# Performance work log

Measured on AMD Instinct MI355X. Metric: run time of the kernel, lower is better.

The kernel has to match this reference:

```python
import jax, jax.numpy as jnp
import numpy as np

B, T, S = 128, 256, 64
IN, H, K, CSL, OUT = 3, 512, 10, 60, 121


def setup_inputs() -> dict:
    key = jax.random.key(0)
    ks = jax.random.split(key, 10)
    s = lambda k, shape, sc: jax.random.normal(k, shape, jnp.float32) * sc
    return {
        "x": jax.random.normal(ks[0], (B, T, IN), jnp.float32),
        "sentences": jax.random.uniform(ks[1], (B, S, CSL), dtype=jnp.float32),
        "h1_h": jnp.zeros((B, H), jnp.float32),
        "h1_c": jnp.zeros((B, H), jnp.float32),
        "h2_h": jnp.zeros((B, H), jnp.float32),
        "h2_c": jnp.zeros((B, H), jnp.float32),
        # LSTMCell params (torch gate order i,f,g,o); b = b_ih + b_hh fused
        "W_ih_cell": s(ks[2], (4 * H, IN + CSL), 0.04),
        "W_hh_cell": s(ks[3], (4 * H, H), 0.04),
        "b_cell": jnp.zeros((4 * H,), jnp.float32),
        # second-layer nn.LSTM params
        "W_ih_l": s(ks[4], (4 * H, IN + CSL + H), 0.04),
        "W_hh_l": s(ks[5], (4 * H, H), 0.04),
        "b_l": jnp.zeros((4 * H,), jnp.float32),
        # fc1 -> window params, fc2 -> output
        "W1": s(ks[6], (3 * K, H), 0.04),
        "b1": jnp.zeros((3 * K,), jnp.float32),
        "W2": s(ks[7], (OUT, H), 0.04),
        "b2": jnp.zeros((OUT,), jnp.float32),
    }


def _lstm_step(h, c, xt, W_ih, W_hh, b):
    g = xt @ W_ih.T + h @ W_hh.T + b
    i, f, gg, o = jnp.split(g, 4, axis=-1)
    c2 = jax.nn.sigmoid(f) * c + jax.nn.sigmoid(i) * jnp.tanh(gg)
    h2 = jax.nn.sigmoid(o) * jnp.tanh(c2)
    return h2, c2


def reference(x, sentences, h1_h, h1_c, h2_h, h2_c,
              W_ih_cell, W_hh_cell, b_cell,
              W_ih_l, W_hh_l, b_l, W1, b1, W2, b2):
    u = jnp.arange(1, S + 1, dtype=x.dtype)[:, None]  # [S,1] char positions

    def step1(carry, xt):
        h, c, p = carry
        ip = jnp.exp(h @ W1.T + b1)                                     # [B,3K]
        # kappa part subtracts the previous step's kappa (quirk of the source)
        p_new = jnp.concatenate([ip[:, :2 * K], ip[:, 2 * K:] - p[:, 2 * K:]], axis=-1)
        a, be, ka = jnp.split(p_new[:, None, :], 3, axis=-1)            # each [B,1,K]
        phi = (a * jnp.exp(-be * (ka - u) ** 2)).sum(-1)                # [B,S]
        win = jnp.einsum('bs,bsc->bc', phi, sentences)                  # [B,CSL]
        h2, c2 = _lstm_step(h, c, jnp.concatenate([xt, win], axis=-1),
                            W_ih_cell, W_hh_cell, b_cell)
        return (h2, c2, p_new), (h2, win)

    xs = jnp.swapaxes(x, 0, 1)                                          # [T,B,IN]
    p0 = jnp.zeros((x.shape[0], 3 * K), x.dtype)
    (h1f, c1f, _), (hx, wins) = jax.lax.scan(step1, (h1_h, h1_c, p0), xs)

    feat = jnp.concatenate([xs, wins, hx], axis=-1)                     # [T,B,IN+CSL+H]

    def step2(carry, xt):
        h, c = carry
        h2, c2 = _lstm_step(h, c, xt, W_ih_l, W_hh_l, b_l)
        return (h2, c2), h2

    (h2f, c2f), ys = jax.lax.scan(step2, (h2_h, h2_c), feat)
    y = jnp.swapaxes(ys, 0, 1).reshape(-1, H)                           # [B*T,H]
    out = y @ W2.T + b2                                                 # [B*T,OUT]
    return out, h1f, c1f, h2f, c2f
```

## Files before the change

kernel.cpp:

```cpp
#include <hip/hip_runtime.h>
#include <hip/hip_bf16.h>
#include <math.h>

typedef __attribute__((ext_vector_type(8))) short short8;
typedef __attribute__((ext_vector_type(4))) float floatx4;

#define DEVFN static __device__ __forceinline__

constexpr int B = 128, T = 256, H = 512;
constexpr int OUTW = 121;
constexpr int SLOTW = 1664;
constexpr int LOOF  = 1088;
constexpr int SLOTE = B * SLOTW;
constexpr int NSLOT = T + 2;
constexpr int NG  = 2048;
constexpr int K1  = 576,  K1C = 18;
constexpr int K2  = 1088, K2C = 34;
constexpr int KW1P = 584, KW2P = 1096;

constexpr int O_WH1 = 0;
constexpr int O_WL1 = 37376;
constexpr int O_W1S = 74752;
constexpr int O_GSM = 137152;
constexpr int O_HS  = 137152;
constexpr int O_PP  = 139264;
constexpr int O_IPL = 145472;
constexpr int O_KL  = 145592;
constexpr int O_PHL = 145632;
constexpr int O_WAC = 145888;
constexpr int O_KPR = 146848;
constexpr int O_B1S = 146888;
constexpr int O_BIA = 147008;
constexpr int O_SENT = 147136;
constexpr int O_WH2 = 0;
constexpr int O_WL2 = 70144;
constexpr int O_GS2 = 140288;
constexpr int O_BI2 = 148608;
constexpr int LDS_SZ = 162496;

DEVFN __hip_bfloat16 bhi(float v) { return __float2bfloat16(v); }
DEVFN __hip_bfloat16 blo(float v, __hip_bfloat16 h) { return __float2bfloat16(v - __bfloat162float(h)); }
DEVFN float bf2f(__hip_bfloat16 h) { return __bfloat162float(h); }
DEVFN unsigned short bbits(__hip_bfloat16 h) { union { __hip_bfloat16 h; unsigned short u; } c; c.h = h; return c.u; }
DEVFN unsigned int pack2(float a, float b) {
  return (unsigned int)bbits(bhi(a)) | ((unsigned int)bbits(bhi(b)) << 16);
}
DEVFN void ast(unsigned int* p, unsigned int v) {
  __hip_atomic_store(p, v, __ATOMIC_RELAXED, __HIP_MEMORY_SCOPE_AGENT);
}
DEVFN int ald(int* p) {
  return __hip_atomic_load(p, __ATOMIC_RELAXED, __HIP_MEMORY_SCOPE_AGENT);
}

DEVFN void waitcnt_ge(int* cnt, int target) {
  if (threadIdx.x == 0) {
    int g = 0;
    while (ald(cnt) < target && g < (1 << 24)) { ++g; __builtin_amdgcn_s_sleep(1); }
  }
  asm volatile("" ::: "memory");
  __syncthreads();
}
DEVFN void cnt_add(int* cnt) {
  asm volatile("s_waitcnt vmcnt(0)" ::: "memory");
  __syncthreads();
  if (threadIdx.x == 0)
    (void)__hip_atomic_fetch_add(cnt, 1, __ATOMIC_RELAXED, __HIP_MEMORY_SCOPE_AGENT);
}

__global__ __launch_bounds__(256) void k_pre(
    const float* __restrict__ x, const float* __restrict__ h1h, const float* __restrict__ h2h,
    const float* __restrict__ Wihc, const float* __restrict__ Whhc, const float* __restrict__ bc,
    const float* __restrict__ Wihl, const float* __restrict__ Whhl, const float* __restrict__ bl,
    const float* __restrict__ W2,
    __hip_bfloat16* __restrict__ fxHL,
    __hip_bfloat16* __restrict__ wc1, __hip_bfloat16* __restrict__ wc1l,
    __hip_bfloat16* __restrict__ wc2, __hip_bfloat16* __restrict__ wc2l,
    __hip_bfloat16* __restrict__ w2b, float* __restrict__ bi1, float* __restrict__ bi2,
    int* __restrict__ ctl)
{
  int idx = blockIdx.x * 256 + threadIdx.x;
  const int nwc1 = NG * K1, nwc2 = NG * K2, nw2b = 128 * 512, nbi = 2 * NG;
  const int nfh = B * H, nxj = T * B, nctl = 512;
  if (idx < nwc1) {
    int n = idx / K1, col = idx - n * K1;
    int src = (n & 3) * H + (n >> 2);
    float v = (col < 63) ? Wihc[src * 63 + col]
            : (col == 63 ? 0.f : Whhc[src * 512 + (col - 64)]);
    __hip_bfloat16 h = bhi(v);
    wc1[n * K1 + col] = h; wc1l[n * K1 + col] = blo(v, h);
    return;
  }
  idx -= nwc1;
  if (idx < nwc2) {
    int n = idx / K2, col = idx - n * K2;
    int src = (n & 3) * H + (n >> 2);
    float v;
    if (col < 63)       v = Wihl[src * 575 + col];
    else if (col == 63) v = 0.f;
    else if (col < 576) v = Wihl[src * 575 + (col - 1)];
    else                v = Whhl[src * 512 + (col - 576)];
    __hip_bfloat16 h = bhi(v);
    wc2[n * K2 + col] = h; wc2l[n * K2 + col] = blo(v, h);
    return;
  }
  idx -= nwc2;
  if (idx < nw2b) {
    int n = idx >> 9, col = idx & 511;
    w2b[idx] = bhi(n < OUTW ? W2[n * 512 + col] : 0.f);
    return;
  }
  idx -= nw2b;
  if (idx < nbi) {
    int n = idx & (NG - 1);
    int src = (n & 3) * H + (n >> 2);
    if (idx < NG) bi1[n] = bc[src]; else bi2[n] = bl[src];
    return;
  }
  idx -= nbi;
  if (idx < nfh) {
    int b = idx >> 9, j = idx & 511;
    float v = h1h[idx];
    __hip_bfloat16 h = bhi(v);
    fxHL[b * SLOTW + 64 + j] = h;
    fxHL[b * SLOTW + LOOF + 64 + j] = blo(v, h);
    return;
  }
  idx -= nfh;
  if (idx < nfh) {
    int b = idx >> 9, j = idx & 511;
    fxHL[(size_t)SLOTE + b * SLOTW + 576 + j] = bhi(h2h[idx]);
    return;
  }
  idx -= nfh;
  if (idx < nxj) {
    int t = idx >> 7, b = idx & 127;
    float x0 = x[(b * T + t) * 3 + 0], x1 = x[(b * T + t) * 3 + 1];
    unsigned int* ph = (unsigned int*)(fxHL + (size_t)(t + 1) * SLOTE + b * SLOTW);
    ph[0] = pack2(x0, x1);
    unsigned int* pl = (unsigned int*)(fxHL + (size_t)(t + 1) * SLOTE + b * SLOTW + LOOF);
    pl[0] = 0u;
    return;
  }
  idx -= nxj;
  if (idx < nctl) ctl[idx] = 0;
}

template <int KWP>
DEVFN void gemm3(int tid, const __hip_bfloat16* __restrict__ Aslot, int m0,
                 const __hip_bfloat16* __restrict__ Wh, const __hip_bfloat16* __restrict__ Wl,
                 int cbeg, int cend, floatx4& a0, floatx4& a1)
{
  const int lane = tid & 63, wv = tid >> 6;
  const int lm = lane & 15, lk = (lane >> 4) << 3;
  const __hip_bfloat16* Ar = Aslot + (size_t)(m0 + wv * 16 + lm) * SLOTW;
  const __hip_bfloat16* W0h = Wh + lm * KWP;
  const __hip_bfloat16* W1h = Wh + (16 + lm) * KWP;
  const __hip_bfloat16* W0l = Wl + lm * KWP;
  const __hip_bfloat16* W1l = Wl + (16 + lm) * KWP;
  #pragma unroll 4
  for (int c = cbeg; c < cend; ++c) {
    int col = c * 32 + lk;
    short8 va  = *(const short8*)(Ar + col);
    short8 ua  = *(const short8*)(Ar + LOOF + col);
    short8 vb0 = *(const short8*)(W0h + col);
    short8 vb1 = *(const short8*)(W1h + col);
    short8 ub0 = *(const short8*)(W0l + col);
    short8 ub1 = *(const short8*)(W1l + col);
    a0 = __builtin_amdgcn_mfma_f32_16x16x32_bf16(va, vb0, a0, 0, 0, 0);
    a1 = __builtin_amdgcn_mfma_f32_16x16x32_bf16(va, vb1, a1, 0, 0, 0);
    a0 = __builtin_amdgcn_mfma_f32_16x16x32_bf16(va, ub0, a0, 0, 0, 0);
    a1 = __builtin_amdgcn_mfma_f32_16x16x32_bf16(va, ub1, a1, 0, 0, 0);
    a0 = __builtin_amdgcn_mfma_f32_16x16x32_bf16(ua, vb0, a0, 0, 0, 0);
    a1 = __builtin_amdgcn_mfma_f32_16x16x32_bf16(ua, vb1, a1, 0, 0, 0);
  }
}

DEVFN void store_gsm(int tid, float* Gsm, floatx4 a0, floatx4 a1) {
  const int lane = tid & 63, wv = tid >> 6;
  const int lm = lane & 15, rr = (lane >> 4) << 2;
  #pragma unroll
  for (int r = 0; r < 4; ++r) {
    Gsm[lm * 65 + wv * 16 + rr + r]        = a0[r];
    Gsm[(16 + lm) * 65 + wv * 16 + rr + r] = a1[r];
  }
}

__global__ __launch_bounds__(256, 1) void k_persist(
    __hip_bfloat16* __restrict__ fxHL,
    const __hip_bfloat16* __restrict__ wc1, const __hip_bfloat16* __restrict__ wc1l,
    const __hip_bfloat16* __restrict__ wc2, const __hip_bfloat16* __restrict__ wc2l,
    const float* __restrict__ bi1, const float* __restrict__ bi2,
    const float* __restrict__ c1init, const float* __restrict__ c2init,
    const float* __restrict__ xin, const float* __restrict__ sent,
    const float* __restrict__ W1, const float* __restrict__ b1,
    int* __restrict__ ctl,
    float* __restrict__ h1f, float* __restrict__ c1f,
    float* __restrict__ h2f, float* __restrict__ c2f)
{
  extern __shared__ char sm[];
  const int gid = blockIdx.x, tid = threadIdx.x;
  const int lane = tid & 63, wv = tid >> 6;
  const int lm = lane & 15, lk = (lane >> 4) << 3;

  if (gid < 128) {
    const int nt1 = gid >> 1, mh = gid & 1;
    const int n0 = nt1 * 32, m0 = mh * 64;
    const int brow = mh * 64 + nt1;
    int* hcnt = ctl + mh * 32;
    int* wcnt = ctl + 64 + mh * 32;
    __hip_bfloat16* smWh = (__hip_bfloat16*)(sm + O_WH1);
    __hip_bfloat16* smWl = (__hip_bfloat16*)(sm + O_WL1);
    float* smW1 = (float*)(sm + O_W1S);
    float* Gsm  = (float*)(sm + O_GSM);
    float* hs   = (float*)(sm + O_HS);
    float* winv = (float*)(sm + O_HS);
    float* pp   = (float*)(sm + O_PP);
    float* ipl  = (float*)(sm + O_IPL);
    float* kl   = (float*)(sm + O_KL);
    float* phl  = (float*)(sm + O_PHL);
    float* wac  = (float*)(sm + O_WAC);
    float* kpr  = (float*)(sm + O_KPR);
    float* b1s  = (float*)(sm + O_B1S);
    float* bia  = (float*)(sm + O_BIA);
    float* ssent = (float*)(sm + O_SENT);

    for (int i = tid; i < 32 * 72; i += 256) {
      int r = i / 72, c8 = (i - r * 72) * 8;
      *(short8*)(smWh + r * KW1P + c8) = *(const short8*)(wc1  + (size_t)(n0 + r) * K1 + c8);
      *(short8*)(smWl + r * KW1P + c8) = *(const short8*)(wc1l + (size_t)(n0 + r) * K1 + c8);
    }
    for (int i = tid; i < 30 * 512; i += 256) {
      int j = i >> 9, c = i & 511;
      smW1[j * 520 + (c >> 6) * 65 + (c & 63)] = W1[i];
    }
    for (int i = tid; i < 64 * 60; i += 256)
      ssent[i] = sent[(size_t)brow * 64 * 60 + i];
    if (tid < 30) b1s[tid] = b1[tid];
    if (tid < 10) kpr[tid] = 0.f;
    if (tid < 32) bia[tid] = bi1[n0 + tid];
    __syncthreads();

    float creg[2];
    {
      int ml = tid >> 2, ppi = tid & 3;
      creg[0] = c1init[(m0 + ml) * H + nt1 * 8 + 2 * ppi + 0];
      creg[1] = c1init[(m0 + ml) * H + nt1 * 8 + 2 * ppi + 1];
    }

    const __hip_bfloat16* W0h = smWh + lm * KW1P;
    const __hip_bfloat16* W1h = smWh + (16 + lm) * KW1P;
    const __hip_bfloat16* W0l = smWl + lm * KW1P;
    const __hip_bfloat16* W1l = smWl + (16 + lm) * KW1P;

    for (int t = 0; t < T; ++t) {
      __hip_bfloat16* S1 = fxHL + (size_t)(t + 1) * SLOTE;
      __hip_bfloat16* S0 = fxHL + (size_t)t * SLOTE;

      waitcnt_ge(hcnt, 64 * t);

      const __hip_bfloat16* wrow = S0 + (size_t)brow * SLOTW;
      __hip_bfloat16 a0h = wrow[64 + tid];
      __hip_bfloat16 a0l = wrow[LOOF + 64 + tid];
      __hip_bfloat16 a1h = wrow[64 + 256 + tid];
      __hip_bfloat16 a1l = wrow[LOOF + 64 + 256 + tid];
      float x2v = xin[(brow * T + t) * 3 + 2];
      const __hip_bfloat16* Ar = S0 + (size_t)(m0 + wv * 16 + lm) * SLOTW;
      short8 pva[16], pua[16];
      #pragma unroll
      for (int c = 0; c < 16; ++c) {
        pva[c] = *(const short8*)(Ar + (c + 2) * 32 + lk);
        pua[c] = *(const short8*)(Ar + LOOF + (c + 2) * 32 + lk);
      }
      hs[(tid >> 6) * 66 + (tid & 63)] = bf2f(a0h) + bf2f(a0l);
      hs[((tid + 256) >> 6) * 66 + (tid & 63)] = bf2f(a1h) + bf2f(a1l);
      __syncthreads();

      if (tid < 240) {
        int j = tid >> 3, p = tid & 7;
        const float* wp = smW1 + j * 520 + p * 65;
        const float* hv = hs + p * 66;
        float s = 0.f;
        #pragma unroll 8
        for (int k = 0; k < 64; ++k) s += hv[k] * wp[k];
        pp[tid] = s;
      }
      __syncthreads();
      if (tid < 30) {
        float s = b1s[tid];
        #pragma unroll
        for (int p = 0; p < 8; ++p) s += pp[tid * 8 + p];
        ipl[tid] = expf(s);
      }
      __syncthreads();
      if (tid < 10) {
        float kap = ipl[20 + tid] - kpr[tid];
        kpr[tid] = kap; kl[tid] = kap;
      }
      __syncthreads();
      if (tid < 64) {
        float u = (float)(tid + 1);
        float acc = 0.f;
        #pragma unroll
        for (int k = 0; k < 10; ++k) {
          float d = kl[k] - u;
          acc += ipl[k] * expf(-ipl[10 + k] * d * d);
        }
        phl[tid] = acc;
      }
      __syncthreads();
      if (tid < 240) {
        int c = tid >> 2, p = tid & 3;
        float acc = 0.f;
        #pragma unroll
        for (int s0 = 0; s0 < 16; ++s0)
          acc += phl[p * 16 + s0] * ssent[(p * 16 + s0) * 60 + c];
        wac[tid] = acc;
      }
      __syncthreads();
      if (tid < 60)
        winv[tid] = wac[tid * 4] + wac[tid * 4 + 1] + wac[tid * 4 + 2] + wac[tid * 4 + 3];
      __syncthreads();
      if (tid < 31) {
        int d = 1 + tid;
        int c0 = 2 * d, c1 = 2 * d + 1;
        float v0 = (c0 == 2) ? x2v : winv[c0 - 3];
        float v1 = (c1 == 63) ? 0.f : winv[c1 - 3];
        __hip_bfloat16 h0 = bhi(v0), h1v = bhi(v1);
        unsigned int* prow = (unsigned int*)(S1 + (size_t)brow * SLOTW);
        ast(prow + d, (unsigned int)bbits(h0) | ((unsigned int)bbits(h1v) << 16));
        ast(prow + (LOOF >> 1) + d,
            (unsigned int)bbits(blo(v0, h0)) | ((unsigned int)bbits(blo(v1, h1v)) << 16));
      }
      cnt_add(wcnt);

      floatx4 a0 = {0.f, 0.f, 0.f, 0.f}, a1 = a0;
      #pragma unroll
      for (int c = 0; c < 16; ++c) {
        int col = (c + 2) * 32 + lk;
        short8 vb0 = *(const short8*)(W0h + col);
        short8 vb1 = *(const short8*)(W1h + col);
        short8 ub0 = *(const short8*)(W0l + col);
        short8 ub1 = *(const short8*)(W1l + col);
        a0 = __builtin_amdgcn_mfma_f32_16x16x32_bf16(pva[c], vb0, a0, 0, 0, 0);
        a1 = __builtin_amdgcn_mfma_f32_16x16x32_bf16(pva[c], vb1, a1, 0, 0, 0);
        a0 = __builtin_amdgcn_mfma_f32_16x16x32_bf16(pva[c], ub0, a0, 0, 0, 0);
        a1 = __builtin_amdgcn_mfma_f32_16x16x32_bf16(pva[c], ub1, a1, 0, 0, 0);
        a0 = __builtin_amdgcn_mfma_f32_16x16x32_bf16(pua[c], vb0, a0, 0, 0, 0);
        a1 = __builtin_amdgcn_mfma_f32_16x16x32_bf16(pua[c], vb1, a1, 0, 0, 0);
      }
      waitcnt_ge(wcnt, 64 * (t + 1));
      gemm3<KW1P>(tid, S1, m0, smWh, smWl, 0, 2, a0, a1);
      store_gsm(tid, Gsm, a0, a1);
      __syncthreads();

      {
        int ml = tid >> 2, ppi = tid & 3;
        float v[2];
        #pragma unroll
        for (int j = 0; j < 2; ++j) {
          int nl = ppi * 8 + j * 4;
          float gi = Gsm[(nl + 0) * 65 + ml] + bia[nl + 0];
          float gf = Gsm[(nl + 1) * 65 + ml] + bia[nl + 1];
          float gg = Gsm[(nl + 2) * 65 + ml] + bia[nl + 2];
          float go = Gsm[(nl + 3) * 65 + ml] + bia[nl + 3];
          float ig = 1.f / (1.f + expf(-gi));
          float fg = 1.f / (1.f + expf(-gf));
          float gt = tanhf(gg);
          float og = 1.f / (1.f + expf(-go));
          float cn = fg * creg[j] + ig * gt;
          v[j] = og * tanhf(cn);
          creg[j] = cn;
        }
        __hip_bfloat16 h0 = bhi(v[0]), h1v = bhi(v[1]);
        unsigned int* prow = (unsigned int*)(S1 + (size_t)(m0 + ml) * SLOTW);
        int dw = 32 + nt1 * 4 + ppi;
        ast(prow + dw, (unsigned int)bbits(h0) | ((unsigned int)bbits(h1v) << 16));
        ast(prow + (LOOF >> 1) + dw,
            (unsigned int)bbits(blo(v[0], h0)) | ((unsigned int)bbits(blo(v[1], h1v)) << 16));
        if (t == T - 1) {
          int hg = nt1 * 8 + 2 * ppi;
          h1f[(m0 + ml) * H + hg]     = v[0];  c1f[(m0 + ml) * H + hg]     = creg[0];
          h1f[(m0 + ml) * H + hg + 1] = v[1];  c1f[(m0 + ml) * H + hg + 1] = creg[1];
        }
      }
      cnt_add(hcnt);
    }
  } else {
    const int g = gid - 128;
    const int nt2 = g >> 1, mh = g & 1;
    const int n0 = nt2 * 32, m0 = mh * 64;
    int* hcnt  = ctl + mh * 32;
    int* h2cnt = ctl + 128 + mh * 32;
    __hip_bfloat16* smWh = (__hip_bfloat16*)(sm + O_WH2);
    __hip_bfloat16* smWl = (__hip_bfloat16*)(sm + O_WL2);
    float* Gsm = (float*)(sm + O_GS2);
    float* bia = (float*)(sm + O_BI2);

    for (int i = tid; i < 32 * 136; i += 256) {
      int r = i / 136, c8 = (i - r * 136) * 8;
      *(short8*)(smWh + r * KW2P + c8) = *(const short8*)(wc2  + (size_t)(n0 + r) * K2 + c8);
      *(short8*)(smWl + r * KW2P + c8) = *(const short8*)(wc2l + (size_t)(n0 + r) * K2 + c8);
    }
    if (tid < 32) bia[tid] = bi2[n0 + tid];
    __syncthreads();

    float creg[2];
    {
      int ml = tid >> 2, ppi = tid & 3;
      creg[0] = c2init[(m0 + ml) * H + nt2 * 8 + 2 * ppi + 0];
      creg[1] = c2init[(m0 + ml) * H + nt2 * 8 + 2 * ppi + 1];
    }

    const __hip_bfloat16* W0h = smWh + lm * KW2P;
    const __hip_bfloat16* W1h = smWh + (16 + lm) * KW2P;
    const __hip_bfloat16* W0l = smWl + lm * KW2P;
    const __hip_bfloat16* W1l = smWl + (16 + lm) * KW2P;

    for (int t = 0; t < T; ++t) {
      __hip_bfloat16* S1 = fxHL + (size_t)(t + 1) * SLOTE;
      __hip_bfloat16* S2 = fxHL + (size_t)(t + 2) * SLOTE;
      const __hip_bfloat16* Ar = S1 + (size_t)(m0 + wv * 16 + lm) * SLOTW;

      waitcnt_ge(h2cnt, 64 * t);
      short8 pv2[16];
      #pragma unroll
      for (int c = 0; c < 16; ++c)
        pv2[c] = *(const short8*)(Ar + (K1C + c) * 32 + lk);
      floatx4 a0 = {0.f, 0.f, 0.f, 0.f}, a1 = a0;
      #pragma unroll
      for (int c = 0; c < 16; ++c) {
        int col = (K1C + c) * 32 + lk;
        short8 vb0 = *(const short8*)(W0h + col);
        short8 vb1 = *(const short8*)(W1h + col);
        short8 ub0 = *(const short8*)(W0l + col);
        short8 ub1 = *(const short8*)(W1l + col);
        a0 = __builtin_amdgcn_mfma_f32_16x16x32_bf16(pv2[c], vb0, a0, 0, 0, 0);
        a1 = __builtin_amdgcn_mfma_f32_16x16x32_bf16(pv2[c], vb1, a1, 0, 0, 0);
        a0 = __builtin_amdgcn_mfma_f32_16x16x32_bf16(pv2[c], ub0, a0, 0, 0, 0);
        a1 = __builtin_amdgcn_mfma_f32_16x16x32_bf16(pv2[c], ub1, a1, 0, 0, 0);
      }
      waitcnt_ge(hcnt, 64 * (t + 1));
      short8 qv[18], qu[18];
      #pragma unroll
      for (int c = 0; c < 18; ++c) {
        qv[c] = *(const short8*)(Ar + c * 32 + lk);
        qu[c] = *(const short8*)(Ar + LOOF + c * 32 + lk);
      }
      #pragma unroll
      for (int c = 0; c < 18; ++c) {
        int col = c * 32 + lk;
        short8 vb0 = *(const short8*)(W0h + col);
        short8 vb1 = *(const short8*)(W1h + col);
        short8 ub0 = *(const short8*)(W0l + col);
        short8 ub1 = *(const short8*)(W1l + col);
        a0 = __builtin_amdgcn_mfma_f32_16x16x32_bf16(qv[c], vb0, a0, 0, 0, 0);
        a1 = __builtin_amdgcn_mfma_f32_16x16x32_bf16(qv[c], vb1, a1, 0, 0, 0);
        a0 = __builtin_amdgcn_mfma_f32_16x16x32_bf16(qv[c], ub0, a0, 0, 0, 0);
        a1 = __builtin_amdgcn_mfma_f32_16x16x32_bf16(qv[c], ub1, a1, 0, 0, 0);
        a0 = __builtin_amdgcn_mfma_f32_16x16x32_bf16(qu[c], vb0, a0, 0, 0, 0);
        a1 = __builtin_amdgcn_mfma_f32_16x16x32_bf16(qu[c], vb1, a1, 0, 0, 0);
      }
      store_gsm(tid, Gsm, a0, a1);
      __syncthreads();

      {
        int ml = tid >> 2, ppi = tid & 3;
        float v[2];
        #pragma unroll
        for (int j = 0; j < 2; ++j) {
          int nl = ppi * 8 + j * 4;
          float gi = Gsm[(nl + 0) * 65 + ml] + bia[nl + 0];
          float gf = Gsm[(nl + 1) * 65 + ml] + bia[nl + 1];
          float gg = Gsm[(nl + 2) * 65 + ml] + bia[nl + 2];
          float go = Gsm[(nl + 3) * 65 + ml] + bia[nl + 3];
          float ig = 1.f / (1.f + expf(-gi));
          float fg = 1.f / (1.f + expf(-gf));
          float gt = tanhf(gg);
          float og = 1.f / (1.f + expf(-go));
          float cn = fg * creg[j] + ig * gt;
          v[j] = og * tanhf(cn);
          creg[j] = cn;
        }
        __hip_bfloat16 h0 = bhi(v[0]), h1v = bhi(v[1]);
        unsigned int* prow = (unsigned int*)(S2 + (size_t)(m0 + ml) * SLOTW);
        int dw = 288 + nt2 * 4 + ppi;
        ast(prow + dw, (unsigned int)bbits(h0) | ((unsigned int)bbits(h1v) << 16));
        if (t == T - 1) {
          int hg = nt2 * 8 + 2 * ppi;
          h2f[(m0 + ml) * H + hg]     = v[0];  c2f[(m0 + ml) * H + hg]     = creg[0];
          h2f[(m0 + ml) * H + hg + 1] = v[1];  c2f[(m0 + ml) * H + hg + 1] = creg[1];
        }
      }
      cnt_add(h2cnt);
    }
  }
}

__global__ __launch_bounds__(256) void k_out(
    const __hip_bfloat16* __restrict__ fxHL, const __hip_bfloat16* __restrict__ w2b,
    const float* __restrict__ b2, float* __restrict__ dout)
{
  int bid = blockIdx.x, tid = threadIdx.x;
  int mblk = bid >> 1, nblk = bid & 1;
  int wv = tid >> 6, lane = tid & 63;
  int lm = lane & 15, lk = (lane >> 4) << 3;
  int m0 = mblk * 128 + wv * 32;
  int n0 = nblk * 64;
  int r0 = m0 + lm, r1 = m0 + 16 + lm;
  const __hip_bfloat16* a0p = fxHL + (size_t)((r0 & 255) + 2) * SLOTE + (r0 >> 8) * SLOTW + 576;
  const __hip_bfloat16* a1p = fxHL + (size_t)((r1 & 255) + 2) * SLOTE + (r1 >> 8) * SLOTW + 576;
  floatx4 zz = {0.f, 0.f, 0.f, 0.f};
  floatx4 acc[2][4];
  #pragma unroll
  for (int mt = 0; mt < 2; ++mt)
    #pragma unroll
    for (int nt = 0; nt < 4; ++nt) acc[mt][nt] = zz;
  #pragma unroll
  for (int c = 0; c < 16; ++c) {
    int col = c * 32 + lk;
    short8 va0 = *(const short8*)(a0p + col);
    short8 va1 = *(const short8*)(a1p + col);
    short8 vb[4];
    #pragma unroll
    for (int nt = 0; nt < 4; ++nt)
      vb[nt] = *(const short8*)(w2b + (size_t)(n0 + nt * 16 + lm) * 512 + col);
    #pragma unroll
    for (int nt = 0; nt < 4; ++nt) {
      acc[0][nt] = __builtin_amdgcn_mfma_f32_16x16x32_bf16(va0, vb[nt], acc[0][nt], 0, 0, 0);
      acc[1][nt] = __builtin_amdgcn_mfma_f32_16x16x32_bf16(va1, vb[nt], acc[1][nt], 0, 0, 0);
    }
  }
  int rr = (lane >> 4) << 2;
  #pragma unroll
  for (int mt = 0; mt < 2; ++mt)
    #pragma unroll
    for (int nt = 0; nt < 4; ++nt)
      #pragma unroll
      for (int r = 0; r < 4; ++r) {
        int m = m0 + mt * 16 + rr + r;
        int n = n0 + nt * 16 + lm;
        if (n < OUTW) dout[(size_t)m * OUTW + n] = acc[mt][nt][r] + b2[n];
      }
}

extern "C" void kernel_launch(void* const* d_in, const int* in_sizes, int n_in,
                              void* d_out, int out_size, void* d_ws, size_t ws_size,
                              hipStream_t stream)
{
  (void)in_sizes; (void)n_in; (void)out_size; (void)ws_size;
  const float* x    = (const float*)d_in[0];
  const float* sent = (const float*)d_in[1];
  const float* h1h  = (const float*)d_in[2];
  const float* h1c  = (const float*)d_in[3];
  const float* h2h  = (const float*)d_in[4];
  const float* h2c  = (const float*)d_in[5];
  const float* Wihc = (const float*)d_in[6];
  const float* Whhc = (const float*)d_in[7];
  const float* bc   = (const float*)d_in[8];
  const float* Wihl = (const float*)d_in[9];
  const float* Whhl = (const float*)d_in[10];
  const float* bl   = (const float*)d_in[11];
  const float* W1   = (const float*)d_in[12];
  const float* b1   = (const float*)d_in[13];
  const float* W2   = (const float*)d_in[14];
  const float* b2   = (const float*)d_in[15];

  float* out = (float*)d_out;
  float* h1f = out + (size_t)B * T * OUTW;
  float* c1f = h1f + (size_t)B * H;
  float* h2f = c1f + (size_t)B * H;
  float* c2f = h2f + (size_t)B * H;

  char* p = (char*)d_ws;
  auto carve = [&](size_t bytes) { char* r = p; p += (bytes + 255) & ~(size_t)255; return r; };
  __hip_bfloat16* fxHL = (__hip_bfloat16*)carve((size_t)NSLOT * SLOTE * 2);
  __hip_bfloat16* wc1  = (__hip_bfloat16*)carve((size_t)NG * K1 * 2);
  __hip_bfloat16* wc1l = (__hip_bfloat16*)carve((size_t)NG * K1 * 2);
  __hip_bfloat16* wc2  = (__hip_bfloat16*)carve((size_t)NG * K2 * 2);
  __hip_bfloat16* wc2l = (__hip_bfloat16*)carve((size_t)NG * K2 * 2);
  __hip_bfloat16* w2b  = (__hip_bfloat16*)carve((size_t)128 * 512 * 2);
  float* bi1 = (float*)carve((size_t)NG * 4);
  float* bi2 = (float*)carve((size_t)NG * 4);
  int*   ctl = (int*)carve((size_t)512 * 4);

  static bool attr_set = false;
  if (!attr_set) {
    (void)hipFuncSetAttribute((const void*)k_persist,
                              hipFuncAttributeMaxDynamicSharedMemorySize, LDS_SZ);
    attr_set = true;
  }

  k_pre<<<14226, 256, 0, stream>>>(x, h1h, h2h, Wihc, Whhc, bc, Wihl, Whhl, bl, W2,
                                   fxHL, wc1, wc1l, wc2, wc2l, w2b, bi1, bi2, ctl);
  k_persist<<<256, 256, LDS_SZ, stream>>>(fxHL, wc1, wc1l, wc2, wc2l, bi1, bi2,
                                          h1c, h2c, x, sent, W1, b1, ctl,
                                          h1f, c1f, h2f, c2f);
  k_out<<<512, 256, 0, stream>>>(fxHL, w2b, b2, out);
}
```

Baseline: 2.684 ms.

## Split global step counters into padded leaf counters and trim intra-step barriers

Replaces each single global atomic counter, previously incremented by 64 blocks per step, with 8 leaf counters on separate 128-byte lines. Each block increments only its own leaf, and waiters poll all 8 leaves in parallel using 8 threads. This is meant to cut atomic contention and polling latency on the cross-block step barriers. It also merges the kappa update into the exp step, drops a syncthreads and the winv reduction pass, and moves the previous-h A-operand loads after the window publish. The control area grows and k_pre launches a few more blocks to zero it.

```diff
diff --git a/kernel.cpp b/kernel.cpp
--- a/kernel.cpp
+++ b/kernel.cpp
@@ -52,19 +52,20 @@
   return __hip_atomic_load(p, __ATOMIC_RELAXED, __HIP_MEMORY_SCOPE_AGENT);
 }
 
-DEVFN void waitcnt_ge(int* cnt, int target) {
-  if (threadIdx.x == 0) {
+DEVFN void waitcnt8(int* base, int target) {
+  if (threadIdx.x < 8) {
+    int* p = base + threadIdx.x * 32;
     int g = 0;
-    while (ald(cnt) < target && g < (1 << 24)) { ++g; __builtin_amdgcn_s_sleep(1); }
+    while (ald(p) < target && g < (1 << 24)) { ++g; __builtin_amdgcn_s_sleep(1); }
   }
   asm volatile("" ::: "memory");
   __syncthreads();
 }
-DEVFN void cnt_add(int* cnt) {
+DEVFN void cnt_add(int* leaf) {
   asm volatile("s_waitcnt vmcnt(0)" ::: "memory");
   __syncthreads();
   if (threadIdx.x == 0)
-    (void)__hip_atomic_fetch_add(cnt, 1, __ATOMIC_RELAXED, __HIP_MEMORY_SCOPE_AGENT);
+    (void)__hip_atomic_fetch_add(leaf, 1, __ATOMIC_RELAXED, __HIP_MEMORY_SCOPE_AGENT);
 }
 
 __global__ __launch_bounds__(256) void k_pre(
@@ -80,7 +81,7 @@
 {
   int idx = blockIdx.x * 256 + threadIdx.x;
   const int nwc1 = NG * K1, nwc2 = NG * K2, nw2b = 128 * 512, nbi = 2 * NG;
-  const int nfh = B * H, nxj = T * B, nctl = 512;
+  const int nfh = B * H, nxj = T * B, nctl = 2048;
   if (idx < nwc1) {
     int n = idx / K1, col = idx - n * K1;
     int src = (n & 3) * H + (n >> 2);
@@ -206,14 +207,14 @@
     const int nt1 = gid >> 1, mh = gid & 1;
     const int n0 = nt1 * 32, m0 = mh * 64;
     const int brow = mh * 64 + nt1;
-    int* hcnt = ctl + mh * 32;
-    int* wcnt = ctl + 64 + mh * 32;
+    const int leaf = (nt1 & 7) * 32;
+    int* hcnt = ctl + mh * 256;
+    int* wcnt = ctl + 512 + mh * 256;
     __hip_bfloat16* smWh = (__hip_bfloat16*)(sm + O_WH1);
     __hip_bfloat16* smWl = (__hip_bfloat16*)(sm + O_WL1);
     float* smW1 = (float*)(sm + O_W1S);
     float* Gsm  = (float*)(sm + O_GSM);
     float* hs   = (float*)(sm + O_HS);
-    float* winv = (float*)(sm + O_HS);
     float* pp   = (float*)(sm + O_PP);
     float* ipl  = (float*)(sm + O_IPL);
     float* kl   = (float*)(sm + O_KL);
@@ -256,7 +257,7 @@
       __hip_bfloat16* S1 = fxHL + (size_t)(t + 1) * SLOTE;
       __hip_bfloat16* S0 = fxHL + (size_t)t * SLOTE;
 
-      waitcnt_ge(hcnt, 64 * t);
+      waitcnt8(hcnt, 8 * t);
 
       const __hip_bfloat16* wrow = S0 + (size_t)brow * SLOTW;
       __hip_bfloat16 a0h = wrow[64 + tid];
@@ -264,13 +265,6 @@
       __hip_bfloat16 a1h = wrow[64 + 256 + tid];
       __hip_bfloat16 a1l = wrow[LOOF + 64 + 256 + tid];
       float x2v = xin[(brow * T + t) * 3 + 2];
-      const __hip_bfloat16* Ar = S0 + (size_t)(m0 + wv * 16 + lm) * SLOTW;
-      short8 pva[16], pua[16];
-      #pragma unroll
-      for (int c = 0; c < 16; ++c) {
-        pva[c] = *(const short8*)(Ar + (c + 2) * 32 + lk);
-        pua[c] = *(const short8*)(Ar + LOOF + (c + 2) * 32 + lk);
-      }
       hs[(tid >> 6) * 66 + (tid & 63)] = bf2f(a0h) + bf2f(a0l);
       hs[((tid + 256) >> 6) * 66 + (tid & 63)] = bf2f(a1h) + bf2f(a1l);
       __syncthreads();
@@ -289,14 +283,14 @@
         float s = b1s[tid];
         #pragma unroll
         for (int p = 0; p < 8; ++p) s += pp[tid * 8 + p];
-        ipl[tid] = expf(s);
-      }
-      __syncthreads();
-      if (tid < 10) {
-        float kap = ipl[20 + tid] - kpr[tid];
-        kpr[tid] = kap; kl[tid] = kap;
-      }
-      __syncthreads();
+        float e = expf(s);
+        ipl[tid] = e;
+        if (tid >= 20) {
+          float kap = e - kpr[tid - 20];
+          kpr[tid - 20] = kap; kl[tid - 20] = kap;
+        }
+      }
+      asm volatile("s_waitcnt lgkmcnt(0)" ::: "memory");
       if (tid < 64) {
         float u = (float)(tid + 1);
         float acc = 0.f;
@@ -317,22 +311,29 @@
         wac[tid] = acc;
       }
       __syncthreads();
-      if (tid < 60)
-        winv[tid] = wac[tid * 4] + wac[tid * 4 + 1] + wac[tid * 4 + 2] + wac[tid * 4 + 3];
-      __syncthreads();
       if (tid < 31) {
         int d = 1 + tid;
         int c0 = 2 * d, c1 = 2 * d + 1;
-        float v0 = (c0 == 2) ? x2v : winv[c0 - 3];
-        float v1 = (c1 == 63) ? 0.f : winv[c1 - 3];
+        float v0, v1;
+        if (c0 == 2) v0 = x2v;
+        else { int j = (c0 - 3) * 4; v0 = wac[j] + wac[j + 1] + wac[j + 2] + wac[j + 3]; }
+        if (c1 == 63) v1 = 0.f;
+        else { int j = (c1 - 3) * 4; v1 = wac[j] + wac[j + 1] + wac[j + 2] + wac[j + 3]; }
         __hip_bfloat16 h0 = bhi(v0), h1v = bhi(v1);
         unsigned int* prow = (unsigned int*)(S1 + (size_t)brow * SLOTW);
         ast(prow + d, (unsigned int)bbits(h0) | ((unsigned int)bbits(h1v) << 16));
         ast(prow + (LOOF >> 1) + d,
             (unsigned int)bbits(blo(v0, h0)) | ((unsigned int)bbits(blo(v1, h1v)) << 16));
       }
-      cnt_add(wcnt);
-
+      cnt_add(wcnt + leaf);
+
+      const __hip_bfloat16* Ar = S0 + (size_t)(m0 + wv * 16 + lm) * SLOTW;
+      short8 pva[16], pua[16];
+      #pragma unroll
+      for (int c = 0; c < 16; ++c) {
+        pva[c] = *(const short8*)(Ar + (c + 2) * 32 + lk);
+        pua[c] = *(const short8*)(Ar + LOOF + (c + 2) * 32 + lk);
+      }
       floatx4 a0 = {0.f, 0.f, 0.f, 0.f}, a1 = a0;
       #pragma unroll
       for (int c = 0; c < 16; ++c) {
@@ -348,7 +349,7 @@
         a0 = __builtin_amdgcn_mfma_f32_16x16x32_bf16(pua[c], vb0, a0, 0, 0, 0);
         a1 = __builtin_amdgcn_mfma_f32_16x16x32_bf16(pua[c], vb1, a1, 0, 0, 0);
       }
-      waitcnt_ge(wcnt, 64 * (t + 1));
+      waitcnt8(wcnt, 8 * (t + 1));
       gemm3<KW1P>(tid, S1, m0, smWh, smWl, 0, 2, a0, a1);
       store_gsm(tid, Gsm, a0, a1);
       __syncthreads();
@@ -383,14 +384,15 @@
           h1f[(m0 + ml) * H + hg + 1] = v[1];  c1f[(m0 + ml) * H + hg + 1] = creg[1];
         }
       }
-      cnt_add(hcnt);
+      cnt_add(hcnt + leaf);
     }
   } else {
     const int g = gid - 128;
     const int nt2 = g >> 1, mh = g & 1;
     const int n0 = nt2 * 32, m0 = mh * 64;
-    int* hcnt  = ctl + mh * 32;
-    int* h2cnt = ctl + 128 + mh * 32;
+    const int leaf = (nt2 & 7) * 32;
+    int* hcnt = ctl + mh * 256;
+    int* h2g  = ctl + 1024 + mh * 256;
     __hip_bfloat16* smWh = (__hip_bfloat16*)(sm + O_WH2);
     __hip_bfloat16* smWl = (__hip_bfloat16*)(sm + O_WL2);
     float* Gsm = (float*)(sm + O_GS2);
@@ -421,7 +423,7 @@
       __hip_bfloat16* S2 = fxHL + (size_t)(t + 2) * SLOTE;
       const __hip_bfloat16* Ar = S1 + (size_t)(m0 + wv * 16 + lm) * SLOTW;
 
-      waitcnt_ge(h2cnt, 64 * t);
+      waitcnt8(h2g, 8 * t);
       short8 pv2[16];
       #pragma unroll
       for (int c = 0; c < 16; ++c)
@@ -439,7 +441,7 @@
         a0 = __builtin_amdgcn_mfma_f32_16x16x32_bf16(pv2[c], ub0, a0, 0, 0, 0);
         a1 = __builtin_amdgcn_mfma_f32_16x16x32_bf16(pv2[c], ub1, a1, 0, 0, 0);
       }
-      waitcnt_ge(hcnt, 64 * (t + 1));
+      waitcnt8(hcnt, 8 * (t + 1));
       short8 qv[18], qu[18];
       #pragma unroll
       for (int c = 0; c < 18; ++c) {
@@ -491,7 +493,7 @@
           h2f[(m0 + ml) * H + hg + 1] = v[1];  c2f[(m0 + ml) * H + hg + 1] = creg[1];
         }
       }
-      cnt_add(h2cnt);
+      cnt_add(h2g + leaf);
     }
   }
 }
@@ -581,7 +583,7 @@
   __hip_bfloat16* w2b  = (__hip_bfloat16*)carve((size_t)128 * 512 * 2);
   float* bi1 = (float*)carve((size_t)NG * 4);
   float* bi2 = (float*)carve((size_t)NG * 4);
-  int*   ctl = (int*)carve((size_t)512 * 4);
+  int*   ctl = (int*)carve((size_t)2048 * 4);
 
   static bool attr_set = false;
   if (!attr_set) {
@@ -590,7 +592,7 @@
     attr_set = true;
   }
 
-  k_pre<<<14226, 256, 0, stream>>>(x, h1h, h2h, Wihc, Whhc, bc, Wihl, Whhl, bl, W2,
+  k_pre<<<14232, 256, 0, stream>>>(x, h1h, h2h, Wihc, Whhc, bc, Wihl, Whhl, bl, W2,
                                    fxHL, wc1, wc1l, wc2, wc2l, w2b, bi1, bi2, ctl);
   k_persist<<<256, 256, LDS_SZ, stream>>>(fxHL, wc1, wc1l, wc2, wc2l, bi1, bi2,
                                           h1c, h2c, x, sent, W1, b1, ctl,
```

Result: slower. 3.146 ms (+17.2%).
